# Optimization experiments

Hardware: AMD Instinct MI355X
Metric: run time of the kernel (lower is better)

## Reference

```python
import jax, jax.numpy as jnp
import numpy as np

EPS = 1e-4

def _hat(v):
    # v: (N,3) -> skew-symmetric (N,3,3)
    x, y, z = v[:, 0], v[:, 1], v[:, 2]
    o = jnp.zeros_like(x)
    r0 = jnp.stack([o, -z, y], axis=-1)
    r1 = jnp.stack([z, o, -x], axis=-1)
    r2 = jnp.stack([-y, x, o], axis=-1)
    return jnp.stack([r0, r1, r2], axis=-2)

def _se3_exp_map(log_transform):
    # log_transform: (N,6) -> (N,4,4)
    log_trans, log_rot = log_transform[:, :3], log_transform[:, 3:]
    skews = _hat(log_rot)                       # (N,3,3)
    skews_sq = jnp.matmul(skews, skews)         # (N,3,3)
    theta = jnp.sqrt(jnp.clip(jnp.sum(log_rot * log_rot, axis=-1), EPS))
    inv = 1.0 / theta
    s, c = jnp.sin(theta), jnp.cos(theta)
    A = (s * inv)[:, None, None]
    B = ((1.0 - c) * inv * inv)[:, None, None]
    C = ((theta - s) * inv * inv * inv)[:, None, None]
    I = jnp.eye(3, dtype=log_transform.dtype)[None]
    R = I + A * skews + B * skews_sq
    V = I + B * skews + C * skews_sq
    T = jnp.einsum('nij,nj->ni', V, log_trans)  # (N,3)
    top = jnp.concatenate([R, T[:, :, None]], axis=-1)  # (N,3,4)
    bottom = jnp.broadcast_to(
        jnp.array([0.0, 0.0, 0.0, 1.0], dtype=log_transform.dtype)[None, None, :],
        (log_transform.shape[0], 1, 4))
    return jnp.concatenate([top, bottom], axis=1)  # (N,4,4)

def setup_inputs() -> dict:
    key = jax.random.key(0)
    k1, k2, k3 = jax.random.split(key, 3)
    B = 2_000_000
    n_views = 2_000_000
    extrinsics = jax.random.normal(k1, (B, 4, 4), dtype=jnp.float32)
    se3_weight = jax.random.normal(k2, (n_views, 6), dtype=jnp.float32)
    indices = jax.random.randint(k3, (B,), 0, n_views, dtype=jnp.int64 if jax.config.jax_enable_x64 else jnp.int32)
    return {"extrinsics": extrinsics, "se3_weight": se3_weight, "indices": indices}

def reference(extrinsics, se3_weight, indices):
    log_transform = se3_weight[indices]          # embedding lookup (B,6)
    refinement = _se3_exp_map(log_transform)     # (B,4,4)
    return jnp.matmul(refinement, extrinsics)    # (B,4,4)
```

## Files before the change

### kernel.cpp

```cpp
#include <hip/hip_runtime.h>

typedef float f32x4 __attribute__((ext_vector_type(4)));

__device__ __forceinline__ int lds_slot(int p) {
    return (p >> 2) * 5 + (p & 3);
}

__global__ __launch_bounds__(256) void se3_apply_g2(
    const float* __restrict__ ext,
    const float* __restrict__ se3,
    const int*   __restrict__ idx,
    float*       __restrict__ out,
    int B, int N)
{
    __shared__ f32x4 lds[1280];
    const int t = threadIdx.x;
    const size_t mbase = (size_t)blockIdx.x * 256;
    const int b  = (int)mbase + t;
    const int cb = (b < B) ? b : (B - 1);

    int j = idx[cb];

    size_t byte  = (size_t)j * 24;
    size_t base  = byte & ~(size_t)15;
    size_t total = (size_t)N * 24;
    if (base + 32 > total) base = total - 32;
    const f32x4* sf = reinterpret_cast<const f32x4*>(
                          reinterpret_cast<const char*>(se3) + base);
    f32x4 q0 = sf[0];
    f32x4 q1 = sf[1];
    bool sh = (byte != base);

    const f32x4* extv = reinterpret_cast<const f32x4*>(ext);
    const size_t fbase = mbase * 4;
    const size_t fmax  = (size_t)B * 4;
    size_t g0 = fbase + t;
    size_t g1 = fbase + t + 256;
    size_t g2 = fbase + t + 512;
    size_t g3 = fbase + t + 768;
    f32x4 s0 = __builtin_nontemporal_load(&extv[g0 < fmax ? g0 : 0]);
    f32x4 s1 = __builtin_nontemporal_load(&extv[g1 < fmax ? g1 : 0]);
    f32x4 s2 = __builtin_nontemporal_load(&extv[g2 < fmax ? g2 : 0]);
    f32x4 s3 = __builtin_nontemporal_load(&extv[g3 < fmax ? g3 : 0]);

    lds[lds_slot(t      )] = s0;
    lds[lds_slot(t + 256)] = s1;
    lds[lds_slot(t + 512)] = s2;
    lds[lds_slot(t + 768)] = s3;
    __syncthreads();

    f32x4 e0 = lds[t*5 + 0];
    f32x4 e1 = lds[t*5 + 1];
    f32x4 e2 = lds[t*5 + 2];
    f32x4 e3 = lds[t*5 + 3];

    float tx = sh ? q0.z : q0.x;
    float ty = sh ? q0.w : q0.y;
    float tz = sh ? q1.x : q0.z;
    float x  = sh ? q1.y : q0.w;
    float y  = sh ? q1.z : q1.x;
    float z  = sh ? q1.w : q1.y;

    float dot   = x*x + y*y + z*z;
    float t2    = fmaxf(dot, 1e-4f);
    float inv   = rsqrtf(t2);
    float theta = t2 * inv;
    float s = __sinf(theta);
    float c = __cosf(theta);
    float A  = s * inv;
    float Bc = (1.0f - c) * inv * inv;
    float Cc = (theta - s) * inv * inv * inv;

    float xx = x*x, yy = y*y, zz = z*z;
    float xy = x*y, xz = x*z, yz = y*z;

    float R00 = 1.0f - Bc*(yy + zz);
    float R01 = -A*z + Bc*xy;
    float R02 =  A*y + Bc*xz;
    float R10 =  A*z + Bc*xy;
    float R11 = 1.0f - Bc*(xx + zz);
    float R12 = -A*x + Bc*yz;
    float R20 = -A*y + Bc*xz;
    float R21 =  A*x + Bc*yz;
    float R22 = 1.0f - Bc*(xx + yy);

    float V00 = 1.0f - Cc*(yy + zz);
    float V01 = -Bc*z + Cc*xy;
    float V02 =  Bc*y + Cc*xz;
    float V10 =  Bc*z + Cc*xy;
    float V11 = 1.0f - Cc*(xx + zz);
    float V12 = -Bc*x + Cc*yz;
    float V20 = -Bc*y + Cc*xz;
    float V21 =  Bc*x + Cc*yz;
    float V22 = 1.0f - Cc*(xx + yy);

    float T0 = V00*tx + V01*ty + V02*tz;
    float T1 = V10*tx + V11*ty + V12*tz;
    float T2 = V20*tx + V21*ty + V22*tz;

    f32x4 o0, o1, o2;
    o0.x = R00*e0.x + R01*e1.x + R02*e2.x + T0*e3.x;
    o0.y = R00*e0.y + R01*e1.y + R02*e2.y + T0*e3.y;
    o0.z = R00*e0.z + R01*e1.z + R02*e2.z + T0*e3.z;
    o0.w = R00*e0.w + R01*e1.w + R02*e2.w + T0*e3.w;

    o1.x = R10*e0.x + R11*e1.x + R12*e2.x + T1*e3.x;
    o1.y = R10*e0.y + R11*e1.y + R12*e2.y + T1*e3.y;
    o1.z = R10*e0.z + R11*e1.z + R12*e2.z + T1*e3.z;
    o1.w = R10*e0.w + R11*e1.w + R12*e2.w + T1*e3.w;

    o2.x = R20*e0.x + R21*e1.x + R22*e2.x + T2*e3.x;
    o2.y = R20*e0.y + R21*e1.y + R22*e2.y + T2*e3.y;
    o2.z = R20*e0.z + R21*e1.z + R22*e2.z + T2*e3.z;
    o2.w = R20*e0.w + R21*e1.w + R22*e2.w + T2*e3.w;

    lds[t*5 + 0] = o0;
    lds[t*5 + 1] = o1;
    lds[t*5 + 2] = o2;
    __syncthreads();

    f32x4* outv = reinterpret_cast<f32x4*>(out);
    if (g0 < fmax) __builtin_nontemporal_store(lds[lds_slot(t      )], &outv[g0]);
    if (g1 < fmax) __builtin_nontemporal_store(lds[lds_slot(t + 256)], &outv[g1]);
    if (g2 < fmax) __builtin_nontemporal_store(lds[lds_slot(t + 512)], &outv[g2]);
    if (g3 < fmax) __builtin_nontemporal_store(lds[lds_slot(t + 768)], &outv[g3]);
}

extern "C" void kernel_launch(void* const* d_in, const int* in_sizes, int n_in,
                              void* d_out, int out_size, void* d_ws, size_t ws_size,
                              hipStream_t stream) {
    const float* ext = (const float*)d_in[0];
    const float* se3 = (const float*)d_in[1];
    const int*   idx = (const int*)d_in[2];
    float* out = (float*)d_out;

    int B = in_sizes[2];
    int N = in_sizes[1] / 6;
    int block = 256;
    int grid = (B + 255) / 256;
    se3_apply_g2<<<grid, block, 0, stream>>>(ext, se3, idx, out, B, N);
}
```

Baseline: 80.38 us.

## Use persistent grid-stride blocks with software-prefetched index and se3 gathers

The one-tile-per-block launch becomes a persistent grid of at most 2048 blocks that stride over 256-element tiles. Each block fetches the next tile's index and se3 row while it computes the current tile, hiding the dependent gather latency. The cost is a smaller grid, which means fewer waves in flight to hide HBM latency on a purely bandwidth-bound streaming kernel. It also adds an extra barrier per iteration and keeps more registers live.

```diff
diff --git a/kernel.cpp b/kernel.cpp
--- a/kernel.cpp
+++ b/kernel.cpp
@@ -6,124 +6,155 @@
     return (p >> 2) * 5 + (p & 3);
 }
 
-__global__ __launch_bounds__(256) void se3_apply_g2(
+__global__ __launch_bounds__(256) void se3_apply_pipe(
     const float* __restrict__ ext,
     const float* __restrict__ se3,
     const int*   __restrict__ idx,
     float*       __restrict__ out,
-    int B, int N)
+    int B, int N, int nt)
 {
     __shared__ f32x4 lds[1280];
     const int t = threadIdx.x;
-    const size_t mbase = (size_t)blockIdx.x * 256;
-    const int b  = (int)mbase + t;
-    const int cb = (b < B) ? b : (B - 1);
+    const size_t total = (size_t)N * 24;
+    const char* se3c = reinterpret_cast<const char*>(se3);
+    const f32x4* extv = reinterpret_cast<const f32x4*>(ext);
+    f32x4* outv = reinterpret_cast<f32x4*>(out);
+    const size_t fmax = (size_t)B * 4;
+    const int stride = gridDim.x;
 
-    int j = idx[cb];
+    int k = blockIdx.x;
+    if (k >= nt) return;
 
-    size_t byte  = (size_t)j * 24;
-    size_t base  = byte & ~(size_t)15;
-    size_t total = (size_t)N * 24;
-    if (base + 32 > total) base = total - 32;
-    const f32x4* sf = reinterpret_cast<const f32x4*>(
-                          reinterpret_cast<const char*>(se3) + base);
-    f32x4 q0 = sf[0];
-    f32x4 q1 = sf[1];
-    bool sh = (byte != base);
+    {
+        int b0 = k * 256 + t;
+        int cb = (b0 < B) ? b0 : (B - 1);
+        int j = idx[cb];
+        size_t byte = (size_t)j * 24;
+        size_t base = byte & ~(size_t)15;
+        if (base + 32 > total) base = total - 32;
+        f32x4 q0 = *reinterpret_cast<const f32x4*>(se3c + base);
+        f32x4 q1 = *reinterpret_cast<const f32x4*>(se3c + base + 16);
+        bool sh = (byte != base);
 
-    const f32x4* extv = reinterpret_cast<const f32x4*>(ext);
-    const size_t fbase = mbase * 4;
-    const size_t fmax  = (size_t)B * 4;
-    size_t g0 = fbase + t;
-    size_t g1 = fbase + t + 256;
-    size_t g2 = fbase + t + 512;
-    size_t g3 = fbase + t + 768;
-    f32x4 s0 = __builtin_nontemporal_load(&extv[g0 < fmax ? g0 : 0]);
-    f32x4 s1 = __builtin_nontemporal_load(&extv[g1 < fmax ? g1 : 0]);
-    f32x4 s2 = __builtin_nontemporal_load(&extv[g2 < fmax ? g2 : 0]);
-    f32x4 s3 = __builtin_nontemporal_load(&extv[g3 < fmax ? g3 : 0]);
+        while (true) {
+            int knext = k + stride;
+            bool have_next = (knext < nt);
 
-    lds[lds_slot(t      )] = s0;
-    lds[lds_slot(t + 256)] = s1;
-    lds[lds_slot(t + 512)] = s2;
-    lds[lds_slot(t + 768)] = s3;
-    __syncthreads();
+            int jn = 0;
+            if (have_next) {
+                int bn = knext * 256 + t;
+                int cbn = (bn < B) ? bn : (B - 1);
+                jn = idx[cbn];
+            }
 
-    f32x4 e0 = lds[t*5 + 0];
-    f32x4 e1 = lds[t*5 + 1];
-    f32x4 e2 = lds[t*5 + 2];
-    f32x4 e3 = lds[t*5 + 3];
+            size_t fbase = (size_t)k * 1024;
+            size_t g0 = fbase + t;
+            size_t g1 = g0 + 256;
+            size_t g2 = g0 + 512;
+            size_t g3 = g0 + 768;
+            f32x4 s0 = __builtin_nontemporal_load(&extv[g0 < fmax ? g0 : 0]);
+            f32x4 s1 = __builtin_nontemporal_load(&extv[g1 < fmax ? g1 : 0]);
+            f32x4 s2 = __builtin_nontemporal_load(&extv[g2 < fmax ? g2 : 0]);
+            f32x4 s3 = __builtin_nontemporal_load(&extv[g3 < fmax ? g3 : 0]);
 
-    float tx = sh ? q0.z : q0.x;
-    float ty = sh ? q0.w : q0.y;
-    float tz = sh ? q1.x : q0.z;
-    float x  = sh ? q1.y : q0.w;
-    float y  = sh ? q1.z : q1.x;
-    float z  = sh ? q1.w : q1.y;
+            __syncthreads();
+            lds[lds_slot(t      )] = s0;
+            lds[lds_slot(t + 256)] = s1;
+            lds[lds_slot(t + 512)] = s2;
+            lds[lds_slot(t + 768)] = s3;
+            __syncthreads();
 
-    float dot   = x*x + y*y + z*z;
-    float t2    = fmaxf(dot, 1e-4f);
-    float inv   = rsqrtf(t2);
-    float theta = t2 * inv;
-    float s = __sinf(theta);
-    float c = __cosf(theta);
-    float A  = s * inv;
-    float Bc = (1.0f - c) * inv * inv;
-    float Cc = (theta - s) * inv * inv * inv;
+            f32x4 e0 = lds[t*5 + 0];
+            f32x4 e1 = lds[t*5 + 1];
+            f32x4 e2 = lds[t*5 + 2];
+            f32x4 e3 = lds[t*5 + 3];
 
-    float xx = x*x, yy = y*y, zz = z*z;
-    float xy = x*y, xz = x*z, yz = y*z;
+            f32x4 nq0 = q0, nq1 = q1;
+            bool nsh = sh;
+            if (have_next) {
+                size_t nbyte = (size_t)jn * 24;
+                size_t nbase = nbyte & ~(size_t)15;
+                if (nbase + 32 > total) nbase = total - 32;
+                nq0 = *reinterpret_cast<const f32x4*>(se3c + nbase);
+                nq1 = *reinterpret_cast<const f32x4*>(se3c + nbase + 16);
+                nsh = (nbyte != nbase);
+            }
 
-    float R00 = 1.0f - Bc*(yy + zz);
-    float R01 = -A*z + Bc*xy;
-    float R02 =  A*y + Bc*xz;
-    float R10 =  A*z + Bc*xy;
-    float R11 = 1.0f - Bc*(xx + zz);
-    float R12 = -A*x + Bc*yz;
-    float R20 = -A*y + Bc*xz;
-    float R21 =  A*x + Bc*yz;
-    float R22 = 1.0f - Bc*(xx + yy);
+            float tx = sh ? q0.z : q0.x;
+            float ty = sh ? q0.w : q0.y;
+            float tz = sh ? q1.x : q0.z;
+            float x  = sh ? q1.y : q0.w;
+            float y  = sh ? q1.z : q1.x;
+            float z  = sh ? q1.w : q1.y;
 
-    float V00 = 1.0f - Cc*(yy + zz);
-    float V01 = -Bc*z + Cc*xy;
-    float V02 =  Bc*y + Cc*xz;
-    float V10 =  Bc*z + Cc*xy;
-    float V11 = 1.0f - Cc*(xx + zz);
-    float V12 = -Bc*x + Cc*yz;
-    float V20 = -Bc*y + Cc*xz;
-    float V21 =  Bc*x + Cc*yz;
-    float V22 = 1.0f - Cc*(xx + yy);
+            float dot   = x*x + y*y + z*z;
+            float t2    = fmaxf(dot, 1e-4f);
+            float inv   = rsqrtf(t2);
+            float theta = t2 * inv;
+            float s = __sinf(theta);
+            float c = __cosf(theta);
+            float A  = s * inv;
+            float Bc = (1.0f - c) * inv * inv;
+            float Cc = (theta - s) * inv * inv * inv;
 
-    float T0 = V00*tx + V01*ty + V02*tz;
-    float T1 = V10*tx + V11*ty + V12*tz;
-    float T2 = V20*tx + V21*ty + V22*tz;
+            float xx = x*x, yy = y*y, zz = z*z;
+            float xy = x*y, xz = x*z, yz = y*z;
 
-    f32x4 o0, o1, o2;
-    o0.x = R00*e0.x + R01*e1.x + R02*e2.x + T0*e3.x;
-    o0.y = R00*e0.y + R01*e1.y + R02*e2.y + T0*e3.y;
-    o0.z = R00*e0.z + R01*e1.z + R02*e2.z + T0*e3.z;
-    o0.w = R00*e0.w + R01*e1.w + R02*e2.w + T0*e3.w;
+            float R00 = 1.0f - Bc*(yy + zz);
+            float R01 = -A*z + Bc*xy;
+            float R02 =  A*y + Bc*xz;
+            float R10 =  A*z + Bc*xy;
+            float R11 = 1.0f - Bc*(xx + zz);
+            float R12 = -A*x + Bc*yz;
+            float R20 = -A*y + Bc*xz;
+            float R21 =  A*x + Bc*yz;
+            float R22 = 1.0f - Bc*(xx + yy);
 
-    o1.x = R10*e0.x + R11*e1.x + R12*e2.x + T1*e3.x;
-    o1.y = R10*e0.y + R11*e1.y + R12*e2.y + T1*e3.y;
-    o1.z = R10*e0.z + R11*e1.z + R12*e2.z + T1*e3.z;
-    o1.w = R10*e0.w + R11*e1.w + R12*e2.w + T1*e3.w;
+            float V00 = 1.0f - Cc*(yy + zz);
+            float V01 = -Bc*z + Cc*xy;
+            float V02 =  Bc*y + Cc*xz;
+            float V10 =  Bc*z + Cc*xy;
+            float V11 = 1.0f - Cc*(xx + zz);
+            float V12 = -Bc*x + Cc*yz;
+            float V20 = -Bc*y + Cc*xz;
+            float V21 =  Bc*x + Cc*yz;
+            float V22 = 1.0f - Cc*(xx + yy);
 
-    o2.x = R20*e0.x + R21*e1.x + R22*e2.x + T2*e3.x;
-    o2.y = R20*e0.y + R21*e1.y + R22*e2.y + T2*e3.y;
-    o2.z = R20*e0.z + R21*e1.z + R22*e2.z + T2*e3.z;
-    o2.w = R20*e0.w + R21*e1.w + R22*e2.w + T2*e3.w;
+            float T0 = V00*tx + V01*ty + V02*tz;
+            float T1 = V10*tx + V11*ty + V12*tz;
+            float T2 = V20*tx + V21*ty + V22*tz;
 
-    lds[t*5 + 0] = o0;
-    lds[t*5 + 1] = o1;
-    lds[t*5 + 2] = o2;
-    __syncthreads();
+            f32x4 o0, o1, o2;
+            o0.x = R00*e0.x + R01*e1.x + R02*e2.x + T0*e3.x;
+            o0.y = R00*e0.y + R01*e1.y + R02*e2.y + T0*e3.y;
+            o0.z = R00*e0.z + R01*e1.z + R02*e2.z + T0*e3.z;
+            o0.w = R00*e0.w + R01*e1.w + R02*e2.w + T0*e3.w;
 
-    f32x4* outv = reinterpret_cast<f32x4*>(out);
-    if (g0 < fmax) __builtin_nontemporal_store(lds[lds_slot(t      )], &outv[g0]);
-    if (g1 < fmax) __builtin_nontemporal_store(lds[lds_slot(t + 256)], &outv[g1]);
-    if (g2 < fmax) __builtin_nontemporal_store(lds[lds_slot(t + 512)], &outv[g2]);
-    if (g3 < fmax) __builtin_nontemporal_store(lds[lds_slot(t + 768)], &outv[g3]);
+            o1.x = R10*e0.x + R11*e1.x + R12*e2.x + T1*e3.x;
+            o1.y = R10*e0.y + R11*e1.y + R12*e2.y + T1*e3.y;
+            o1.z = R10*e0.z + R11*e1.z + R12*e2.z + T1*e3.z;
+            o1.w = R10*e0.w + R11*e1.w + R12*e2.w + T1*e3.w;
+
+            o2.x = R20*e0.x + R21*e1.x + R22*e2.x + T2*e3.x;
+            o2.y = R20*e0.y + R21*e1.y + R22*e2.y + T2*e3.y;
+            o2.z = R20*e0.z + R21*e1.z + R22*e2.z + T2*e3.z;
+            o2.w = R20*e0.w + R21*e1.w + R22*e2.w + T2*e3.w;
+
+            lds[t*5 + 0] = o0;
+            lds[t*5 + 1] = o1;
+            lds[t*5 + 2] = o2;
+            __syncthreads();
+
+            if (g0 < fmax) __builtin_nontemporal_store(lds[lds_slot(t      )], &outv[g0]);
+            if (g1 < fmax) __builtin_nontemporal_store(lds[lds_slot(t + 256)], &outv[g1]);
+            if (g2 < fmax) __builtin_nontemporal_store(lds[lds_slot(t + 512)], &outv[g2]);
+            if (g3 < fmax) __builtin_nontemporal_store(lds[lds_slot(t + 768)], &outv[g3]);
+
+            if (!have_next) break;
+            k = knext;
+            q0 = nq0; q1 = nq1; sh = nsh;
+        }
+    }
 }
 
 extern "C" void kernel_launch(void* const* d_in, const int* in_sizes, int n_in,
@@ -136,7 +167,7 @@
 
     int B = in_sizes[2];
     int N = in_sizes[1] / 6;
-    int block = 256;
-    int grid = (B + 255) / 256;
-    se3_apply_g2<<<grid, block, 0, stream>>>(ext, se3, idx, out, B, N);
+    int nt = (B + 255) / 256;
+    int grid = nt < 2048 ? nt : 2048;
+    se3_apply_pipe<<<grid, 256, 0, stream>>>(ext, se3, idx, out, B, N, nt);
 }
```

Result: slower. 82.56 us (+2.7%).

## Use four threads per matrix with DPP quad permutes instead of LDS transpose

Applied to the files above, without the earlier changes.

Each output 4x4 matrix is now handled by four lanes, one per row. Each lane loads one contiguous row of extrinsics and exchanges rows with its neighbours through DPP quad permutes, so the product needs no LDS staging and no barriers. This removes the shared-memory round trips and both __syncthreads. In exchange, the index and se3 gather and the exp-map math are repeated by all four lanes of a quad, and four times as many threads are launched.

```diff
diff --git a/kernel.cpp b/kernel.cpp
--- a/kernel.cpp
+++ b/kernel.cpp
@@ -2,57 +2,48 @@
 
 typedef float f32x4 __attribute__((ext_vector_type(4)));
 
-__device__ __forceinline__ int lds_slot(int p) {
-    return (p >> 2) * 5 + (p & 3);
+template<int CTRL>
+__device__ __forceinline__ float qperm(float v) {
+    int i = __builtin_bit_cast(int, v);
+    i = __builtin_amdgcn_update_dpp(0, i, CTRL, 0xF, 0xF, true);
+    return __builtin_bit_cast(float, i);
 }
 
-__global__ __launch_bounds__(256) void se3_apply_g2(
+template<int CTRL>
+__device__ __forceinline__ f32x4 qperm4(f32x4 v) {
+    f32x4 r;
+    r.x = qperm<CTRL>(v.x);
+    r.y = qperm<CTRL>(v.y);
+    r.z = qperm<CTRL>(v.z);
+    r.w = qperm<CTRL>(v.w);
+    return r;
+}
+
+__global__ __launch_bounds__(256) void se3_apply_quad(
     const float* __restrict__ ext,
     const float* __restrict__ se3,
     const int*   __restrict__ idx,
     float*       __restrict__ out,
     int B, int N)
 {
-    __shared__ f32x4 lds[1280];
-    const int t = threadIdx.x;
-    const size_t mbase = (size_t)blockIdx.x * 256;
-    const int b  = (int)mbase + t;
-    const int cb = (b < B) ? b : (B - 1);
+    const long tid = (long)blockIdx.x * 256 + threadIdx.x;
+    const long m   = tid >> 2;
+    const int  r   = (int)(tid & 3);
+    if (m >= B) return;
 
-    int j = idx[cb];
+    int j = idx[m];
+
+    const f32x4* extv = reinterpret_cast<const f32x4*>(ext);
+    f32x4 E = __builtin_nontemporal_load(&extv[tid]);
 
     size_t byte  = (size_t)j * 24;
     size_t base  = byte & ~(size_t)15;
     size_t total = (size_t)N * 24;
     if (base + 32 > total) base = total - 32;
-    const f32x4* sf = reinterpret_cast<const f32x4*>(
-                          reinterpret_cast<const char*>(se3) + base);
-    f32x4 q0 = sf[0];
-    f32x4 q1 = sf[1];
+    const char* se3c = reinterpret_cast<const char*>(se3);
+    f32x4 q0 = *reinterpret_cast<const f32x4*>(se3c + base);
+    f32x4 q1 = *reinterpret_cast<const f32x4*>(se3c + base + 16);
     bool sh = (byte != base);
-
-    const f32x4* extv = reinterpret_cast<const f32x4*>(ext);
-    const size_t fbase = mbase * 4;
-    const size_t fmax  = (size_t)B * 4;
-    size_t g0 = fbase + t;
-    size_t g1 = fbase + t + 256;
-    size_t g2 = fbase + t + 512;
-    size_t g3 = fbase + t + 768;
-    f32x4 s0 = __builtin_nontemporal_load(&extv[g0 < fmax ? g0 : 0]);
-    f32x4 s1 = __builtin_nontemporal_load(&extv[g1 < fmax ? g1 : 0]);
-    f32x4 s2 = __builtin_nontemporal_load(&extv[g2 < fmax ? g2 : 0]);
-    f32x4 s3 = __builtin_nontemporal_load(&extv[g3 < fmax ? g3 : 0]);
-
-    lds[lds_slot(t      )] = s0;
-    lds[lds_slot(t + 256)] = s1;
-    lds[lds_slot(t + 512)] = s2;
-    lds[lds_slot(t + 768)] = s3;
-    __syncthreads();
-
-    f32x4 e0 = lds[t*5 + 0];
-    f32x4 e1 = lds[t*5 + 1];
-    f32x4 e2 = lds[t*5 + 2];
-    f32x4 e3 = lds[t*5 + 3];
 
     float tx = sh ? q0.z : q0.x;
     float ty = sh ? q0.w : q0.y;
@@ -74,56 +65,41 @@
     float xx = x*x, yy = y*y, zz = z*z;
     float xy = x*y, xz = x*z, yz = y*z;
 
-    float R00 = 1.0f - Bc*(yy + zz);
-    float R01 = -A*z + Bc*xy;
-    float R02 =  A*y + Bc*xz;
-    float R10 =  A*z + Bc*xy;
-    float R11 = 1.0f - Bc*(xx + zz);
-    float R12 = -A*x + Bc*yz;
-    float R20 = -A*y + Bc*xz;
-    float R21 =  A*x + Bc*yz;
-    float R22 = 1.0f - Bc*(xx + yy);
+    bool r0 = (r == 0), r1 = (r == 1), r2 = (r == 2), r3 = (r == 3);
+    float kr0 = r1 ?  z : r2 ? -y : 0.0f;
+    float kr1 = r0 ? -z : r2 ?  x : 0.0f;
+    float kr2 = r0 ?  y : r1 ? -x : 0.0f;
+    float k20 = r0 ? -(yy + zz) : r1 ? xy : r2 ? xz : 0.0f;
+    float k21 = r0 ? xy : r1 ? -(xx + zz) : r2 ? yz : 0.0f;
+    float k22 = r0 ? xz : r1 ? yz : r2 ? -(xx + yy) : 0.0f;
+    float d0 = r0 ? 1.0f : 0.0f;
+    float d1 = r1 ? 1.0f : 0.0f;
+    float d2 = r2 ? 1.0f : 0.0f;
 
-    float V00 = 1.0f - Cc*(yy + zz);
-    float V01 = -Bc*z + Cc*xy;
-    float V02 =  Bc*y + Cc*xz;
-    float V10 =  Bc*z + Cc*xy;
-    float V11 = 1.0f - Cc*(xx + zz);
-    float V12 = -Bc*x + Cc*yz;
-    float V20 = -Bc*y + Cc*xz;
-    float V21 =  Bc*x + Cc*yz;
-    float V22 = 1.0f - Cc*(xx + yy);
+    float R0 = d0 + A*kr0 + Bc*k20;
+    float R1 = d1 + A*kr1 + Bc*k21;
+    float R2 = d2 + A*kr2 + Bc*k22;
+    float V0 = d0 + Bc*kr0 + Cc*k20;
+    float V1 = d1 + Bc*kr1 + Cc*k21;
+    float V2 = d2 + Bc*kr2 + Cc*k22;
+    float T  = V0*tx + V1*ty + V2*tz;
 
-    float T0 = V00*tx + V01*ty + V02*tz;
-    float T1 = V10*tx + V11*ty + V12*tz;
-    float T2 = V20*tx + V21*ty + V22*tz;
+    float m0 = R0, m1 = R1, m2 = R2;
+    float m3 = r3 ? 1.0f : T;
 
-    f32x4 o0, o1, o2;
-    o0.x = R00*e0.x + R01*e1.x + R02*e2.x + T0*e3.x;
-    o0.y = R00*e0.y + R01*e1.y + R02*e2.y + T0*e3.y;
-    o0.z = R00*e0.z + R01*e1.z + R02*e2.z + T0*e3.z;
-    o0.w = R00*e0.w + R01*e1.w + R02*e2.w + T0*e3.w;
+    float c0 = r0 ? m0 : r1 ? m1 : r2 ? m2 : m3;
+    float c1 = r0 ? m1 : r1 ? m2 : r2 ? m3 : m0;
+    float c2 = r0 ? m2 : r1 ? m3 : r2 ? m0 : m1;
+    float c3 = r0 ? m3 : r1 ? m0 : r2 ? m1 : m2;
 
-    o1.x = R10*e0.x + R11*e1.x + R12*e2.x + T1*e3.x;
-    o1.y = R10*e0.y + R11*e1.y + R12*e2.y + T1*e3.y;
-    o1.z = R10*e0.z + R11*e1.z + R12*e2.z + T1*e3.z;
-    o1.w = R10*e0.w + R11*e1.w + R12*e2.w + T1*e3.w;
+    f32x4 E1 = qperm4<0x39>(E);
+    f32x4 E2 = qperm4<0x4E>(E);
+    f32x4 E3 = qperm4<0x93>(E);
 
-    o2.x = R20*e0.x + R21*e1.x + R22*e2.x + T2*e3.x;
-    o2.y = R20*e0.y + R21*e1.y + R22*e2.y + T2*e3.y;
-    o2.z = R20*e0.z + R21*e1.z + R22*e2.z + T2*e3.z;
-    o2.w = R20*e0.w + R21*e1.w + R22*e2.w + T2*e3.w;
-
-    lds[t*5 + 0] = o0;
-    lds[t*5 + 1] = o1;
-    lds[t*5 + 2] = o2;
-    __syncthreads();
+    f32x4 o = c0*E + c1*E1 + c2*E2 + c3*E3;
 
     f32x4* outv = reinterpret_cast<f32x4*>(out);
-    if (g0 < fmax) __builtin_nontemporal_store(lds[lds_slot(t      )], &outv[g0]);
-    if (g1 < fmax) __builtin_nontemporal_store(lds[lds_slot(t + 256)], &outv[g1]);
-    if (g2 < fmax) __builtin_nontemporal_store(lds[lds_slot(t + 512)], &outv[g2]);
-    if (g3 < fmax) __builtin_nontemporal_store(lds[lds_slot(t + 768)], &outv[g3]);
+    __builtin_nontemporal_store(o, &outv[tid]);
 }
 
 extern "C" void kernel_launch(void* const* d_in, const int* in_sizes, int n_in,
@@ -136,7 +112,7 @@
 
     int B = in_sizes[2];
     int N = in_sizes[1] / 6;
-    int block = 256;
-    int grid = (B + 255) / 256;
-    se3_apply_g2<<<grid, block, 0, stream>>>(ext, se3, idx, out, B, N);
+    long threads = (long)B * 4;
+    int grid = (int)((threads + 255) / 256);
+    se3_apply_quad<<<grid, 256, 0, stream>>>(ext, se3, idx, out, B, N);
 }
```

New measurement: 79.30 us. About the same (-1.3%).
